# Performance work log

Measured on AMD Instinct MI355X. Metric: run time of the kernel, lower is better.

## Reference

```python
import jax, jax.numpy as jnp
import numpy as np

B, T, D, H = 4, 2048, 1024, 16
DH = D // H          # 64
HALF = DH // 2       # 32


def _rope_tables(T, half, base=10000.0):
    inv_freq = 1.0 / (base ** (np.arange(half, dtype=np.float32) / half))
    t = np.arange(T, dtype=np.float32)
    ang = np.outer(t, inv_freq)                       # [T, half]
    cos = jnp.asarray(np.cos(ang))[None, None]        # [1,1,T,half]
    sin = jnp.asarray(np.sin(ang))[None, None]
    return cos, sin


def setup_inputs() -> dict:
    key = jax.random.key(0)
    kx, kq, kp = jax.random.split(key, 3)
    cos, sin = _rope_tables(T, HALF)
    return {
        "x": jax.random.normal(kx, (B, T, D), dtype=jnp.float32),
        "cos": cos,
        "sin": sin,
        "W_qkv": jax.random.normal(kq, (3 * D, D), dtype=jnp.float32) * (D ** -0.5),
        "W_proj": jax.random.normal(kp, (D, D), dtype=jnp.float32) * (D ** -0.5),
    }


def _apply_rope(q, k, cos, sin):
    # q,k: [B,H,T,dh]; cos,sin: [1,1,T,dh/2]
    t = q.shape[2]
    c, s = cos[:, :, :t, :], sin[:, :, :t, :]
    h = q.shape[-1] // 2
    q1, q2 = q[..., :h], q[..., h:]
    k1, k2 = k[..., :h], k[..., h:]
    q_rot = jnp.concatenate([q1 * c - q2 * s, q1 * s + q2 * c], axis=-1)
    k_rot = jnp.concatenate([k1 * c - k2 * s, k1 * s + k2 * c], axis=-1)
    return q_rot, k_rot


def reference(x, cos, sin, W_qkv, W_proj):
    Bb, Tt, C = x.shape
    qkv = x @ W_qkv.T                                 # [B,T,3C]
    q, k, v = jnp.split(qkv, 3, axis=2)
    # [B,T,C] -> [B,H,T,dh]
    q = q.reshape(Bb, Tt, H, DH).transpose(0, 2, 1, 3)
    k = k.reshape(Bb, Tt, H, DH).transpose(0, 2, 1, 3)
    v = v.reshape(Bb, Tt, H, DH).transpose(0, 2, 1, 3)
    q, k = _apply_rope(q, k, cos, sin)
    w = jnp.einsum("bhqd,bhkd->bhqk", q, k) * (DH ** -0.5)
    causal = jnp.tril(jnp.ones((Tt, Tt), dtype=bool))
    w = jnp.where(causal, w, -jnp.inf)
    w = jax.nn.softmax(w.astype(jnp.float32), axis=-1).astype(x.dtype)
    out = jnp.einsum("bhqk,bhkd->bhqd", w, v)
    # XSA: subtract self-value contribution (diagonal attention weight)
    self_w = jnp.diagonal(w, axis1=-2, axis2=-1)[..., None]  # [B,H,T,1]
    out = out - self_w * v
    out = out.transpose(0, 2, 1, 3).reshape(Bb, Tt, C)
    return out @ W_proj.T
```

## Files before the change

### kernel.cpp

```cpp
#include <hip/hip_runtime.h>

constexpr int Tq = 2048;
constexpr int Dq = 1024;

typedef __bf16 bf16x8 __attribute__((ext_vector_type(8)));
typedef float f32x4 __attribute__((ext_vector_type(4)));
typedef _Float16 f16;
typedef f16 f16x4 __attribute__((ext_vector_type(4)));
typedef unsigned short u16;
typedef u16 u16x4 __attribute__((ext_vector_type(4)));
typedef u16 u16x8 __attribute__((ext_vector_type(8)));

__device__ __forceinline__ u16 f2bf(float f) {
    unsigned int u = __float_as_uint(f);
    u += 0x7fffu + ((u >> 16) & 1u);
    return (u16)(u >> 16);
}

__device__ __forceinline__ void gld_lds16(const void* g, void* l) {
    __builtin_amdgcn_global_load_lds(
        (const __attribute__((address_space(1))) unsigned int*)g,
        (__attribute__((address_space(3))) unsigned int*)l, 16, 0, 0);
}

__global__ void cvt3_f32_bf16(const float* __restrict__ a, u16* __restrict__ oa, int na,
                              const float* __restrict__ b, u16* __restrict__ ob, int nb,
                              const float* __restrict__ c, u16* __restrict__ oc, int nc) {
    int i = blockIdx.x * 256 + threadIdx.x;
    const float* in; u16* out;
    if (i < na) { in = a; out = oa; }
    else if (i < na + nb) { in = b; out = ob; i -= na; }
    else if (i < na + nb + nc) { in = c; out = oc; i -= na + nb; }
    else return;
    float4 v = ((const float4*)in)[i];
    u16x4 o;
    o.x = f2bf(v.x); o.y = f2bf(v.y); o.z = f2bf(v.z); o.w = f2bf(v.w);
    ((u16x4*)out)[i] = o;
}

__global__ __launch_bounds__(256) void gemm_qkv(const u16* __restrict__ A,
                                                const u16* __restrict__ B,
                                                const float* __restrict__ cosT,
                                                const float* __restrict__ sinT,
                                                u16* __restrict__ Qb,
                                                u16* __restrict__ Kb,
                                                f16* __restrict__ Vtg) {
    constexpr int K = 1024, N = 3072;
    __shared__ u16 As[128 * 32];
    __shared__ u16 Bs[128 * 32];
    const int t = threadIdx.x;
    const int lane = t & 63;
    const int wave = t >> 6;
    const int l16 = lane & 15;
    const int quad = lane >> 4;
    const int bm = blockIdx.x * 128;
    const int by = blockIdx.y;
    const int bn = by * 128;
    const int wm = (wave & 1) * 64;
    const int wn = (wave >> 1) * 64;
    const int srow = t >> 2;
    const int scol = (t & 3) * 8;

    f32x4 acc[4][4] = {};

    const u16* Ab = A + (size_t)(bm + srow) * K + scol;
    const u16* Bb = B + (size_t)(bn + srow) * K + scol;

    for (int k0 = 0; k0 < K; k0 += 32) {
        gld_lds16(Ab + k0,                    (char*)As + t * 16);
        gld_lds16(Ab + (size_t)64 * K + k0,   (char*)As + 4096 + t * 16);
        gld_lds16(Bb + k0,                    (char*)Bs + t * 16);
        gld_lds16(Bb + (size_t)64 * K + k0,   (char*)Bs + 4096 + t * 16);
        __syncthreads();

        bf16x8 af[4], bf[4];
#pragma unroll
        for (int i = 0; i < 4; i++) {
            af[i] = *(const bf16x8*)&As[(wm + i * 16 + l16) * 32 + quad * 8];
            bf[i] = *(const bf16x8*)&Bs[(wn + i * 16 + l16) * 32 + quad * 8];
        }
#pragma unroll
        for (int i = 0; i < 4; i++)
#pragma unroll
            for (int j = 0; j < 4; j++)
                acc[i][j] = __builtin_amdgcn_mfma_f32_16x16x32_bf16(af[i], bf[j], acc[i][j], 0, 0, 0);
        __syncthreads();
    }

    const int kind = by >> 3;
    if (kind < 2) {
        u16* Out = kind ? Kb : Qb;
        const float qscale = kind ? 1.f : 0.18033688011112042f;
        const int h = ((by & 7) << 1) + (wn >> 6);
#pragma unroll
        for (int i = 0; i < 4; i++)
#pragma unroll
            for (int r = 0; r < 4; r++) {
                const int gm = bm + wm + i * 16 + quad * 4 + r;
                const int b = gm >> 11, tt = gm & 2047;
                const size_t row = ((size_t)(b * 16 + h) * Tq + tt) * 64;
#pragma unroll
                for (int jj = 0; jj < 2; jj++) {
                    const int dd = jj * 16 + l16;
                    const float c = cosT[tt * 32 + dd];
                    const float s = sinT[tt * 32 + dd];
                    const float v1 = acc[i][jj][r];
                    const float v2 = acc[i][jj + 2][r];
                    Out[row + dd]      = f2bf((v1 * c - v2 * s) * qscale);
                    Out[row + dd + 32] = f2bf((v1 * s + v2 * c) * qscale);
                }
            }
    } else {
#pragma unroll
        for (int i = 0; i < 4; i++) {
            const int gm0 = bm + wm + i * 16 + quad * 4;
            const int b = gm0 >> 11, tt = gm0 & 2047;
#pragma unroll
            for (int j = 0; j < 4; j++) {
                const int col = wn + j * 16 + l16;
                const int h = ((by & 7) << 1) + (col >> 6);
                const int d = col & 63;
                f16x4 o = {(f16)acc[i][j][0], (f16)acc[i][j][1],
                           (f16)acc[i][j][2], (f16)acc[i][j][3]};
                *(f16x4*)&Vtg[((size_t)(b * 16 + h) * 64 + d) * Tq + tt] = o;
            }
        }
    }
}

__global__ __launch_bounds__(256) void gemm_bt(const u16* __restrict__ A,
                                               const u16* __restrict__ B,
                                               float* __restrict__ Cv,
                                               int M, int N, int K) {
    __shared__ u16 As[128 * 32];
    __shared__ u16 Bs[128 * 32];
    const int t = threadIdx.x;
    const int lane = t & 63;
    const int wave = t >> 6;
    const int l16 = lane & 15;
    const int quad = lane >> 4;
    const int bm = blockIdx.x * 128;
    const int bn = blockIdx.y * 128;
    const int wm = (wave & 1) * 64;
    const int wn = (wave >> 1) * 64;
    const int srow = t >> 2;
    const int scol = (t & 3) * 8;

    f32x4 acc[4][4] = {};

    const u16* Ab = A + (size_t)(bm + srow) * K + scol;
    const u16* Bb = B + (size_t)(bn + srow) * K + scol;

    for (int k0 = 0; k0 < K; k0 += 32) {
        gld_lds16(Ab + k0,                    (char*)As + t * 16);
        gld_lds16(Ab + (size_t)64 * K + k0,   (char*)As + 4096 + t * 16);
        gld_lds16(Bb + k0,                    (char*)Bs + t * 16);
        gld_lds16(Bb + (size_t)64 * K + k0,   (char*)Bs + 4096 + t * 16);
        __syncthreads();

        bf16x8 af[4], bf[4];
#pragma unroll
        for (int i = 0; i < 4; i++) {
            af[i] = *(const bf16x8*)&As[(wm + i * 16 + l16) * 32 + quad * 8];
            bf[i] = *(const bf16x8*)&Bs[(wn + i * 16 + l16) * 32 + quad * 8];
        }
#pragma unroll
        for (int i = 0; i < 4; i++)
#pragma unroll
            for (int j = 0; j < 4; j++)
                acc[i][j] = __builtin_amdgcn_mfma_f32_16x16x32_bf16(af[i], bf[j], acc[i][j], 0, 0, 0);
        __syncthreads();
    }

#pragma unroll
    for (int i = 0; i < 4; i++)
#pragma unroll
        for (int j = 0; j < 4; j++)
#pragma unroll
            for (int r = 0; r < 4; r++) {
                const int gm = bm + wm + i * 16 + quad * 4 + r;
                const int gn = bn + wn + j * 16 + l16;
                Cv[(size_t)gm * N + gn] = acc[i][j][r];
            }
}

template <bool MASK>
__device__ __forceinline__ void flash_tile(const u16* __restrict__ Ks,
                                           const f16* __restrict__ Vs,
                                           const bf16x8& qf0, const bf16x8& qf1,
                                           int l16, int quad, int i_loc,
                                           float& l_run, f32x4* o_acc) {
    f32x4 s[4];
    const int cp0 = quad ^ (l16 & 7);
    const int cp1 = (4 + quad) ^ (l16 & 7);
    __builtin_amdgcn_s_setprio(1);
#pragma unroll
    for (int tn = 0; tn < 4; tn++) {
        const int jrow = tn * 16 + l16;
        bf16x8 kf0 = *(const bf16x8*)&Ks[jrow * 64 + cp0 * 8];
        bf16x8 kf1 = *(const bf16x8*)&Ks[jrow * 64 + cp1 * 8];
        f32x4 z = {0.f, 0.f, 0.f, 0.f};
        z = __builtin_amdgcn_mfma_f32_16x16x32_bf16(kf0, qf0, z, 0, 0, 0);
        z = __builtin_amdgcn_mfma_f32_16x16x32_bf16(kf1, qf1, z, 0, 0, 0);
        s[tn] = z;
    }
    __builtin_amdgcn_s_setprio(0);
    float rsa[4];
#pragma unroll
    for (int tn = 0; tn < 4; tn++) {
        float rs = 0.f;
#pragma unroll
        for (int r = 0; r < 4; r++) {
            float v = s[tn][r];
            if (MASK) {
                const int j_loc = tn * 16 + quad * 4 + r;
                if (j_loc > i_loc) v = -1e30f;
            }
            float p = exp2f(v);
            rs += p;
            if (MASK) {
                const int j_loc = tn * 16 + quad * 4 + r;
                if (j_loc == i_loc) p = 0.f;
            }
            s[tn][r] = p;
        }
        rsa[tn] = rs;
    }
    l_run += (rsa[0] + rsa[1]) + (rsa[2] + rsa[3]);

    f16x4 pf[4];
#pragma unroll
    for (int tk = 0; tk < 4; tk++)
        pf[tk] = f16x4{(f16)s[tk][0], (f16)s[tk][1], (f16)s[tk][2], (f16)s[tk][3]};
    __builtin_amdgcn_s_setprio(1);
#pragma unroll
    for (int td = 0; td < 4; td++) {
        const int drow = td * 16 + l16;
#pragma unroll
        for (int tk = 0; tk < 4; tk++) {
            const int cp = (2 * tk + (quad >> 1)) ^ (l16 & 7);
            f16x4 vf = *(const f16x4*)&Vs[drow * 64 + cp * 8 + (quad & 1) * 4];
            o_acc[td] = __builtin_amdgcn_mfma_f32_16x16x16f16(vf, pf[tk], o_acc[td], 0, 0, 0);
        }
    }
    __builtin_amdgcn_s_setprio(0);
}

__global__ __launch_bounds__(512, 4) void flash(const u16* __restrict__ Qb,
                                                const u16* __restrict__ Kb,
                                                const f16* __restrict__ Vtg,
                                                u16* __restrict__ Ob) {
    __shared__ __align__(16) char smem[65536];

    const int t = threadIdx.x, lane = t & 63, wave = t >> 6;
    const int l16 = lane & 15, quad = lane >> 4;
    const int i = blockIdx.x;
    const int xcd = i & 7, w = i >> 3;
    const int bh = xcd * 8 + (w >> 4);
    const int b = bh >> 4, h = bh & 15;
    const int x = w & 15;
    const int qt = (wave < 4) ? x : (31 - x);
    const int q0w = qt * 64;
    const u16* Qp = Qb + (size_t)bh * Tq * 64;
    const u16* Kp = Kb + (size_t)bh * Tq * 64;
    const f16* Vp = Vtg + (size_t)bh * 64 * Tq;

    const int i_abs = q0w + (wave & 3) * 16 + l16;
    bf16x8 qf0 = *(const bf16x8*)(Qp + (size_t)i_abs * 64 + quad * 8);
    bf16x8 qf1 = *(const bf16x8*)(Qp + (size_t)i_abs * 64 + 32 + quad * 8);
    asm volatile("s_waitcnt vmcnt(0)" : "+v"(qf0), "+v"(qf1) :: "memory");

    float l_run = 0.f;
    f32x4 o_acc[4] = {};

    const int srow = t >> 3;
    const int sc = (t & 7) ^ (srow & 7);
    const int diag_n = qt;
    const int i_tloc = (wave & 3) * 16 + l16;
    const int nt = 32 - x;
    const int nt2 = (nt + 1) >> 1;

    auto stage = [&](int n2) {
        const int j0 = n2 * 128;
        char* buf = smem + (n2 & 1) * 32768;
        gld_lds16(Kp + (size_t)(j0 + srow) * 64 + sc * 8,      buf + t * 16);
        gld_lds16(Kp + (size_t)(j0 + 64 + srow) * 64 + sc * 8, buf + 8192 + t * 16);
        gld_lds16(Vp + (size_t)srow * Tq + j0 + sc * 8,        buf + 16384 + t * 16);
        gld_lds16(Vp + (size_t)srow * Tq + j0 + 64 + sc * 8,   buf + 24576 + t * 16);
    };

    stage(0);
    for (int n2 = 0; n2 < nt2; n2++) {
        asm volatile("s_waitcnt vmcnt(0)\n\ts_barrier" ::: "memory");
        if (n2 + 1 < nt2) stage(n2 + 1);
        char* cb = smem + (n2 & 1) * 32768;
#pragma unroll
        for (int s = 0; s < 2; s++) {
            const int tile = n2 * 2 + s;
            const u16* Ks = (const u16*)(cb + s * 8192);
            const f16* Vs = (const f16*)(cb + 16384 + s * 8192);
            if (tile < diag_n)
                flash_tile<false>(Ks, Vs, qf0, qf1, l16, quad, i_tloc, l_run, o_acc);
            else if (tile == diag_n)
                flash_tile<true>(Ks, Vs, qf0, qf1, l16, quad, i_tloc, l_run, o_acc);
        }
    }

    l_run += __shfl_xor(l_run, 16, 64);
    l_run += __shfl_xor(l_run, 32, 64);
    const float inv_l = 1.f / l_run;

    __syncthreads();
    u16* Os = (u16*)smem;
#pragma unroll
    for (int td = 0; td < 4; td++) {
        u16x4 o;
#pragma unroll
        for (int r = 0; r < 4; r++) o[r] = f2bf(o_acc[td][r] * inv_l);
        *(u16x4*)&Os[wave * 1152 + l16 * 72 + td * 16 + quad * 4] = o;
    }
    __syncthreads();
    const int oi = lane >> 2, od = (lane & 3) * 16;
    u16x8 r0 = *(const u16x8*)&Os[wave * 1152 + oi * 72 + od];
    u16x8 r1 = *(const u16x8*)&Os[wave * 1152 + oi * 72 + od + 8];
    const size_t orow = ((size_t)b * Tq + q0w + (wave & 3) * 16 + oi) * Dq + h * 64 + od;
    *(u16x8*)&Ob[orow] = r0;
    *(u16x8*)&Ob[orow + 8] = r1;
}

extern "C" void kernel_launch(void* const* d_in, const int* in_sizes, int n_in,
                              void* d_out, int out_size, void* d_ws, size_t ws_size,
                              hipStream_t stream) {
    const float* x     = (const float*)d_in[0];
    const float* cosT  = (const float*)d_in[1];
    const float* sinT  = (const float*)d_in[2];
    const float* Wqkv  = (const float*)d_in[3];
    const float* Wproj = (const float*)d_in[4];

    u16* xb     = (u16*)d_ws;
    u16* wqkvb  = xb + (size_t)8192 * 1024;
    u16* wprojb = wqkvb + (size_t)3072 * 1024;
    u16* Qb     = wprojb + (size_t)1024 * 1024;
    u16* Kb     = Qb + (size_t)64 * 2048 * 64;
    f16* Vtg    = (f16*)(Kb + (size_t)64 * 2048 * 64);
    u16* attn   = (u16*)(Vtg + (size_t)64 * 64 * 2048);

    cvt3_f32_bf16<<<12288, 256, 0, stream>>>(x, xb, 2097152,
                                             Wqkv, wqkvb, 786432,
                                             Wproj, wprojb, 262144);

    gemm_qkv<<<dim3(64, 24), 256, 0, stream>>>(xb, wqkvb, cosT, sinT, Qb, Kb, Vtg);
    flash<<<1024, 512, 0, stream>>>(Qb, Kb, Vtg, attn);
    gemm_bt<<<dim3(64, 8), 256, 0, stream>>>(attn, wprojb, (float*)d_out, 8192, 1024, 1024);
}
```

Before: 263.0 us.

## Process both paired query tiles per wave in flash kernel with 256 threads

The flash kernel drops from 512 to 256 threads per block. Each wave now holds Q fragments and accumulators for both the early and late query tiles, so every K/V tile staged in shared memory feeds two query tiles from the same registers. This improves reuse of each staged K/V tile and halves the thread count, but it doubles the accumulator registers per wave. The launch bounds drop to 2 blocks per CU, which may lower occupancy and latency hiding.

```diff
diff --git a/kernel.cpp b/kernel.cpp
--- a/kernel.cpp
+++ b/kernel.cpp
@@ -246,7 +246,7 @@
     __builtin_amdgcn_s_setprio(0);
 }
 
-__global__ __launch_bounds__(512, 4) void flash(const u16* __restrict__ Qb,
+__global__ __launch_bounds__(256, 2) void flash(const u16* __restrict__ Qb,
                                                 const u16* __restrict__ Kb,
                                                 const f16* __restrict__ Vtg,
                                                 u16* __restrict__ Ob) {
@@ -259,34 +259,40 @@
     const int bh = xcd * 8 + (w >> 4);
     const int b = bh >> 4, h = bh & 15;
     const int x = w & 15;
-    const int qt = (wave < 4) ? x : (31 - x);
-    const int q0w = qt * 64;
+    const int qtA = x, qtB = 31 - x;
+    const int q0a = qtA * 64, q0b = qtB * 64;
     const u16* Qp = Qb + (size_t)bh * Tq * 64;
     const u16* Kp = Kb + (size_t)bh * Tq * 64;
     const f16* Vp = Vtg + (size_t)bh * 64 * Tq;
 
-    const int i_abs = q0w + (wave & 3) * 16 + l16;
-    bf16x8 qf0 = *(const bf16x8*)(Qp + (size_t)i_abs * 64 + quad * 8);
-    bf16x8 qf1 = *(const bf16x8*)(Qp + (size_t)i_abs * 64 + 32 + quad * 8);
-    asm volatile("s_waitcnt vmcnt(0)" : "+v"(qf0), "+v"(qf1) :: "memory");
-
-    float l_run = 0.f;
-    f32x4 o_acc[4] = {};
-
-    const int srow = t >> 3;
-    const int sc = (t & 7) ^ (srow & 7);
-    const int diag_n = qt;
-    const int i_tloc = (wave & 3) * 16 + l16;
+    const int rowi = wave * 16 + l16;
+    bf16x8 qa0 = *(const bf16x8*)(Qp + (size_t)(q0a + rowi) * 64 + quad * 8);
+    bf16x8 qa1 = *(const bf16x8*)(Qp + (size_t)(q0a + rowi) * 64 + 32 + quad * 8);
+    bf16x8 qb0 = *(const bf16x8*)(Qp + (size_t)(q0b + rowi) * 64 + quad * 8);
+    bf16x8 qb1 = *(const bf16x8*)(Qp + (size_t)(q0b + rowi) * 64 + 32 + quad * 8);
+    asm volatile("s_waitcnt vmcnt(0)"
+                 : "+v"(qa0), "+v"(qa1), "+v"(qb0), "+v"(qb1) :: "memory");
+
+    float lA = 0.f, lB = 0.f;
+    f32x4 oA[4] = {}, oB[4] = {};
+
+    const int sr = t >> 3;
+    const int sc = (t & 7) ^ (sr & 7);
+    const int i_tloc = wave * 16 + l16;
     const int nt = 32 - x;
     const int nt2 = (nt + 1) >> 1;
 
     auto stage = [&](int n2) {
         const int j0 = n2 * 128;
         char* buf = smem + (n2 & 1) * 32768;
-        gld_lds16(Kp + (size_t)(j0 + srow) * 64 + sc * 8,      buf + t * 16);
-        gld_lds16(Kp + (size_t)(j0 + 64 + srow) * 64 + sc * 8, buf + 8192 + t * 16);
-        gld_lds16(Vp + (size_t)srow * Tq + j0 + sc * 8,        buf + 16384 + t * 16);
-        gld_lds16(Vp + (size_t)srow * Tq + j0 + 64 + sc * 8,   buf + 24576 + t * 16);
+        gld_lds16(Kp + (size_t)(j0 + sr) * 64 + sc * 8,            buf + t * 16);
+        gld_lds16(Kp + (size_t)(j0 + 32 + sr) * 64 + sc * 8,       buf + 4096 + t * 16);
+        gld_lds16(Kp + (size_t)(j0 + 64 + sr) * 64 + sc * 8,       buf + 8192 + t * 16);
+        gld_lds16(Kp + (size_t)(j0 + 96 + sr) * 64 + sc * 8,       buf + 12288 + t * 16);
+        gld_lds16(Vp + (size_t)sr * Tq + j0 + sc * 8,              buf + 16384 + t * 16);
+        gld_lds16(Vp + (size_t)(32 + sr) * Tq + j0 + sc * 8,       buf + 20480 + t * 16);
+        gld_lds16(Vp + (size_t)sr * Tq + j0 + 64 + sc * 8,         buf + 24576 + t * 16);
+        gld_lds16(Vp + (size_t)(32 + sr) * Tq + j0 + 64 + sc * 8,  buf + 28672 + t * 16);
     };
 
     stage(0);
@@ -299,33 +305,52 @@
             const int tile = n2 * 2 + s;
             const u16* Ks = (const u16*)(cb + s * 8192);
             const f16* Vs = (const f16*)(cb + 16384 + s * 8192);
-            if (tile < diag_n)
-                flash_tile<false>(Ks, Vs, qf0, qf1, l16, quad, i_tloc, l_run, o_acc);
-            else if (tile == diag_n)
-                flash_tile<true>(Ks, Vs, qf0, qf1, l16, quad, i_tloc, l_run, o_acc);
-        }
-    }
-
-    l_run += __shfl_xor(l_run, 16, 64);
-    l_run += __shfl_xor(l_run, 32, 64);
-    const float inv_l = 1.f / l_run;
+            if (tile < qtB)
+                flash_tile<false>(Ks, Vs, qb0, qb1, l16, quad, i_tloc, lB, oB);
+            else if (tile == qtB)
+                flash_tile<true>(Ks, Vs, qb0, qb1, l16, quad, i_tloc, lB, oB);
+            if (tile < qtA)
+                flash_tile<false>(Ks, Vs, qa0, qa1, l16, quad, i_tloc, lA, oA);
+            else if (tile == qtA)
+                flash_tile<true>(Ks, Vs, qa0, qa1, l16, quad, i_tloc, lA, oA);
+        }
+    }
+
+    lA += __shfl_xor(lA, 16, 64);
+    lA += __shfl_xor(lA, 32, 64);
+    lB += __shfl_xor(lB, 16, 64);
+    lB += __shfl_xor(lB, 32, 64);
+    const float ivA = 1.f / lA, ivB = 1.f / lB;
 
     __syncthreads();
     u16* Os = (u16*)smem;
 #pragma unroll
     for (int td = 0; td < 4; td++) {
-        u16x4 o;
-#pragma unroll
-        for (int r = 0; r < 4; r++) o[r] = f2bf(o_acc[td][r] * inv_l);
-        *(u16x4*)&Os[wave * 1152 + l16 * 72 + td * 16 + quad * 4] = o;
+        u16x4 oa, ob;
+#pragma unroll
+        for (int r = 0; r < 4; r++) {
+            oa[r] = f2bf(oA[td][r] * ivA);
+            ob[r] = f2bf(oB[td][r] * ivB);
+        }
+        *(u16x4*)&Os[wave * 1152 + l16 * 72 + td * 16 + quad * 4] = oa;
+        *(u16x4*)&Os[(4 + wave) * 1152 + l16 * 72 + td * 16 + quad * 4] = ob;
     }
     __syncthreads();
     const int oi = lane >> 2, od = (lane & 3) * 16;
-    u16x8 r0 = *(const u16x8*)&Os[wave * 1152 + oi * 72 + od];
-    u16x8 r1 = *(const u16x8*)&Os[wave * 1152 + oi * 72 + od + 8];
-    const size_t orow = ((size_t)b * Tq + q0w + (wave & 3) * 16 + oi) * Dq + h * 64 + od;
-    *(u16x8*)&Ob[orow] = r0;
-    *(u16x8*)&Ob[orow + 8] = r1;
+    {
+        u16x8 r0 = *(const u16x8*)&Os[wave * 1152 + oi * 72 + od];
+        u16x8 r1 = *(const u16x8*)&Os[wave * 1152 + oi * 72 + od + 8];
+        const size_t orow = ((size_t)b * Tq + q0a + wave * 16 + oi) * Dq + h * 64 + od;
+        *(u16x8*)&Ob[orow] = r0;
+        *(u16x8*)&Ob[orow + 8] = r1;
+    }
+    {
+        u16x8 r0 = *(const u16x8*)&Os[(4 + wave) * 1152 + oi * 72 + od];
+        u16x8 r1 = *(const u16x8*)&Os[(4 + wave) * 1152 + oi * 72 + od + 8];
+        const size_t orow = ((size_t)b * Tq + q0b + wave * 16 + oi) * Dq + h * 64 + od;
+        *(u16x8*)&Ob[orow] = r0;
+        *(u16x8*)&Ob[orow + 8] = r1;
+    }
 }
 
 extern "C" void kernel_launch(void* const* d_in, const int* in_sizes, int n_in,
@@ -350,6 +375,6 @@
                                              Wproj, wprojb, 262144);
 
     gemm_qkv<<<dim3(64, 24), 256, 0, stream>>>(xb, wqkvb, cosT, sinT, Qb, Kb, Vtg);
-    flash<<<1024, 512, 0, stream>>>(Qb, Kb, Vtg, attn);
+    flash<<<1024, 256, 0, stream>>>(Qb, Kb, Vtg, attn);
     gemm_bt<<<dim3(64, 8), 256, 0, stream>>>(attn, wprojb, (float*)d_out, 8192, 1024, 1024);
 }
```

Result: slower. 269.7 us (+2.5%).
